# Kernel tuning notes

Hardware: AMD Instinct MI355X
Metric: run time of the kernel (lower is better)

The kernel has to match this reference:

```python
import jax, jax.numpy as jnp
import numpy as np

FILTER_ORDER = 49   # M
FRAME_PERIOD = 80   # P
IGNORE_GAIN = False


def linear_interpolation(b, P):
    """Upsample frame-level coeffs (..., N, D) -> (..., N*P, D).

    Matches diffsptk LinearInterpolation: replicate-pad last frame, then
    linear interpolation with align_corners=True, i.e.
    h[n*P + p] = (1 - p/P) * b[n] + (p/P) * b[min(n+1, N-1)].
    """
    if P == 1:
        return b
    N, D = b.shape[-2], b.shape[-1]
    left = b                                             # (..., N, D)
    right = jnp.concatenate([b[..., 1:, :], b[..., -1:, :]], axis=-2)  # (..., N, D)
    w = (jnp.arange(P, dtype=b.dtype) / P)[:, None]      # (P, 1)
    h = left[..., :, None, :] * (1 - w) + right[..., :, None, :] * w  # (..., N, P, D)
    return h.reshape(*b.shape[:-2], N * P, D)


def setup_inputs() -> dict:
    key = jax.random.key(0)
    k1, k2 = jax.random.split(key)
    B = 8
    N = 3000                       # number of frames
    T = N * FRAME_PERIOD           # 240000 samples
    x = jax.random.normal(k1, (B, T), dtype=jnp.float32)
    b = jax.random.normal(k2, (B, N, FILTER_ORDER + 1), dtype=jnp.float32)
    return {"x": x, "b": b}


def reference(x, b):
    M = b.shape[-1] - 1
    T = x.shape[-1]
    # per-sample filter taps, flipped so h[..., k] multiplies x[t - M + k]
    h = linear_interpolation(jnp.flip(b, axis=-1), FRAME_PERIOD)  # (B, T, M+1)
    if IGNORE_GAIN:
        h = h / h[..., -1:]
    xp = jnp.pad(x, ((0, 0), (M, 0)))                    # (B, T+M)
    idx = jnp.arange(T)[:, None] + jnp.arange(M + 1)[None, :]  # (T, M+1)
    windows = xp[:, idx]                                 # (B, T, M+1)
    y = jnp.sum(windows * h, axis=-1)                    # (B, T)
    return y
```

## Files before the change

kernel.cpp:

```cpp
#include <hip/hip_runtime.h>

constexpr int M      = 49;
constexpr int TAPS   = 50;
constexpr int P      = 80;
constexpr int BLOCK  = 256;
constexpr int R      = 8;
constexpr int TILE   = BLOCK * R;
constexpr int NFR    = 28;
constexpr int FSTRIDE = 52;

__global__ __launch_bounds__(BLOCK) void azdf_kernel(
    const float* __restrict__ x, const float* __restrict__ b,
    float* __restrict__ y, int T, int N) {
  __shared__ float xs[TILE + M + 15];
  __shared__ float bs[NFR * FSTRIDE];

  const int batch = blockIdx.y;
  const int t0 = blockIdx.x * TILE;
  const int tid = threadIdx.x;
  const float* xb = x + (size_t)batch * T;
  const float* bb = b + (size_t)batch * N * TAPS;

  for (int i = tid; i < TILE + M; i += BLOCK) {
    int xi = t0 - M + i;
    xs[i] = (xi >= 0 && xi < T) ? xb[xi] : 0.0f;
  }
  if (tid < 15) xs[TILE + M + tid] = 0.0f;

  const int n_first = t0 / P;
  for (int i = tid; i < NFR * TAPS; i += BLOCK) {
    int f = i / TAPS;
    int k = i - f * TAPS;
    int n = n_first + f;
    if (n > N - 1) n = N - 1;
    bs[f * FSTRIDE + k] = bb[(size_t)n * TAPS + k];
  }
  __syncthreads();

  const int t_base = t0 + tid * R;
  if (t_base >= T) return;

  float xr[60];
#pragma unroll
  for (int j = 0; j < 15; ++j) {
    float4 v = *(const float4*)&xs[tid * R + 4 * j];
    xr[4 * j + 0] = v.x; xr[4 * j + 1] = v.y;
    xr[4 * j + 2] = v.z; xr[4 * j + 3] = v.w;
  }

  const int n = t_base / P;
  const float* c0 = &bs[(n - n_first) * FSTRIDE];
  const float* c1 = c0 + FSTRIDE;

  float s0[R], s1[R];
#pragma unroll
  for (int r = 0; r < R; ++r) { s0[r] = 0.0f; s1[r] = 0.0f; }

#pragma unroll
  for (int kc = 0; kc < 48; kc += 4) {
    float4 a0 = *(const float4*)&c0[kc];
    float4 a1 = *(const float4*)&c1[kc];
    const float av0[4] = {a0.x, a0.y, a0.z, a0.w};
    const float av1[4] = {a1.x, a1.y, a1.z, a1.w};
#pragma unroll
    for (int kk = 0; kk < 4; ++kk) {
      const int k = kc + kk;
#pragma unroll
      for (int r = 0; r < R; ++r) {
        float xv = xr[M + r - k];
        s0[r] = fmaf(xv, av0[kk], s0[r]);
        s1[r] = fmaf(xv, av1[kk], s1[r]);
      }
    }
  }
  {
    float2 a0 = *(const float2*)&c0[48];
    float2 a1 = *(const float2*)&c1[48];
#pragma unroll
    for (int r = 0; r < R; ++r) {
      float xv = xr[M + r - 48];
      s0[r] = fmaf(xv, a0.x, s0[r]);
      s1[r] = fmaf(xv, a1.x, s1[r]);
    }
#pragma unroll
    for (int r = 0; r < R; ++r) {
      float xv = xr[M + r - 49];
      s0[r] = fmaf(xv, a0.y, s0[r]);
      s1[r] = fmaf(xv, a1.y, s1[r]);
    }
  }

  const int phase = t_base - n * P;
  float out[R];
#pragma unroll
  for (int r = 0; r < R; ++r) {
    float w = (float)(phase + r) * (1.0f / (float)P);
    out[r] = (1.0f - w) * s0[r] + w * s1[r];
  }

  float* yp = y + (size_t)batch * T + t_base;
  if (t_base + R <= T) {
    *(float4*)(yp + 0) = make_float4(out[0], out[1], out[2], out[3]);
    *(float4*)(yp + 4) = make_float4(out[4], out[5], out[6], out[7]);
  } else {
    for (int r = 0; r < R && t_base + r < T; ++r) yp[r] = out[r];
  }
}

extern "C" void kernel_launch(void* const* d_in, const int* in_sizes, int n_in,
                              void* d_out, int out_size, void* d_ws, size_t ws_size,
                              hipStream_t stream) {
  const float* x = (const float*)d_in[0];
  const float* b = (const float*)d_in[1];
  float* y = (float*)d_out;

  const int B = 8;
  const int N = in_sizes[1] / (B * TAPS);
  const int T = N * P;

  dim3 grid((T + TILE - 1) / TILE, B);
  azdf_kernel<<<grid, BLOCK, 0, stream>>>(x, b, y, T, N);
}
```

Baseline: 75.44 us.

## Load x windows directly from global and stage coefficients per wave without barrier

Drops the block-wide shared-memory staging of the input signal. Each thread now reads its 60-sample window straight from global memory with float4 loads and leans on the caches for the overlap between neighbouring threads. Filter-coefficient frames are staged per wavefront into private LDS slices, which removes the __syncthreads barrier, and the store tail guard is dropped because T is assumed to be a multiple of 8. The trade-offs are redundant global/L1 traffic for overlapping x windows, plus reliance on lockstep execution within a wave for LDS visibility without an explicit barrier.

```diff
diff --git a/kernel.cpp b/kernel.cpp
--- a/kernel.cpp
+++ b/kernel.cpp
@@ -5,51 +5,55 @@
 constexpr int P      = 80;
 constexpr int BLOCK  = 256;
 constexpr int R      = 8;
-constexpr int TILE   = BLOCK * R;
-constexpr int NFR    = 28;
+constexpr int WFR    = 9;
 constexpr int FSTRIDE = 52;
+constexpr int WAVES  = BLOCK / 64;
 
 __global__ __launch_bounds__(BLOCK) void azdf_kernel(
     const float* __restrict__ x, const float* __restrict__ b,
     float* __restrict__ y, int T, int N) {
-  __shared__ float xs[TILE + M + 15];
-  __shared__ float bs[NFR * FSTRIDE];
+  __shared__ float bs[WAVES * WFR * FSTRIDE];
 
   const int batch = blockIdx.y;
-  const int t0 = blockIdx.x * TILE;
-  const int tid = threadIdx.x;
+  const int tid  = threadIdx.x;
+  const int wave = tid >> 6;
+  const int lane = tid & 63;
   const float* xb = x + (size_t)batch * T;
   const float* bb = b + (size_t)batch * N * TAPS;
 
-  for (int i = tid; i < TILE + M; i += BLOCK) {
-    int xi = t0 - M + i;
-    xs[i] = (xi >= 0 && xi < T) ? xb[xi] : 0.0f;
-  }
-  if (tid < 15) xs[TILE + M + tid] = 0.0f;
+  const int w0 = (blockIdx.x * BLOCK + wave * 64) * R;
+  const int n_first = w0 / P;
+  float* wbs = &bs[wave * WFR * FSTRIDE];
 
-  const int n_first = t0 / P;
-  for (int i = tid; i < NFR * TAPS; i += BLOCK) {
+  for (int i = lane; i < WFR * TAPS; i += 64) {
     int f = i / TAPS;
     int k = i - f * TAPS;
     int n = n_first + f;
     if (n > N - 1) n = N - 1;
-    bs[f * FSTRIDE + k] = bb[(size_t)n * TAPS + k];
+    wbs[f * FSTRIDE + k] = bb[(size_t)n * TAPS + k];
   }
-  __syncthreads();
 
-  const int t_base = t0 + tid * R;
+  const int t_base = w0 + lane * R;
   if (t_base >= T) return;
 
   float xr[60];
+  if (t_base >= 52) {
+    const float* xp = xb + t_base - 52;
 #pragma unroll
-  for (int j = 0; j < 15; ++j) {
-    float4 v = *(const float4*)&xs[tid * R + 4 * j];
-    xr[4 * j + 0] = v.x; xr[4 * j + 1] = v.y;
-    xr[4 * j + 2] = v.z; xr[4 * j + 3] = v.w;
+    for (int j = 0; j < 15; ++j) {
+      float4 v = *(const float4*)(xp + 4 * j);
+      xr[4*j+0] = v.x; xr[4*j+1] = v.y; xr[4*j+2] = v.z; xr[4*j+3] = v.w;
+    }
+  } else {
+#pragma unroll
+    for (int i = 0; i < 60; ++i) {
+      int xi = t_base - 52 + i;
+      xr[i] = (xi >= 0) ? xb[xi] : 0.0f;
+    }
   }
 
   const int n = t_base / P;
-  const float* c0 = &bs[(n - n_first) * FSTRIDE];
+  const float* c0 = &wbs[(n - n_first) * FSTRIDE];
   const float* c1 = c0 + FSTRIDE;
 
   float s0[R], s1[R];
@@ -67,7 +71,7 @@
       const int k = kc + kk;
 #pragma unroll
       for (int r = 0; r < R; ++r) {
-        float xv = xr[M + r - k];
+        float xv = xr[52 + r - k];
         s0[r] = fmaf(xv, av0[kk], s0[r]);
         s1[r] = fmaf(xv, av1[kk], s1[r]);
       }
@@ -78,13 +82,13 @@
     float2 a1 = *(const float2*)&c1[48];
 #pragma unroll
     for (int r = 0; r < R; ++r) {
-      float xv = xr[M + r - 48];
+      float xv = xr[52 + r - 48];
       s0[r] = fmaf(xv, a0.x, s0[r]);
       s1[r] = fmaf(xv, a1.x, s1[r]);
     }
 #pragma unroll
     for (int r = 0; r < R; ++r) {
-      float xv = xr[M + r - 49];
+      float xv = xr[52 + r - 49];
       s0[r] = fmaf(xv, a0.y, s0[r]);
       s1[r] = fmaf(xv, a1.y, s1[r]);
     }
@@ -99,12 +103,8 @@
   }
 
   float* yp = y + (size_t)batch * T + t_base;
-  if (t_base + R <= T) {
-    *(float4*)(yp + 0) = make_float4(out[0], out[1], out[2], out[3]);
-    *(float4*)(yp + 4) = make_float4(out[4], out[5], out[6], out[7]);
-  } else {
-    for (int r = 0; r < R && t_base + r < T; ++r) yp[r] = out[r];
-  }
+  *(float4*)(yp + 0) = make_float4(out[0], out[1], out[2], out[3]);
+  *(float4*)(yp + 4) = make_float4(out[4], out[5], out[6], out[7]);
 }
 
 extern "C" void kernel_launch(void* const* d_in, const int* in_sizes, int n_in,
@@ -118,6 +118,7 @@
   const int N = in_sizes[1] / (B * TAPS);
   const int T = N * P;
 
-  dim3 grid((T + TILE - 1) / TILE, B);
+  const int threads_per_batch = T / R;
+  dim3 grid((threads_per_batch + BLOCK - 1) / BLOCK, B);
   azdf_kernel<<<grid, BLOCK, 0, stream>>>(x, b, y, T, N);
 }
```

New measurement: 71.46 us. 1.06x faster.
